# Performance work log

Measured on AMD Instinct MI355X. Metric: run time of the kernel, lower is better.

## Reference

```python
import jax, jax.numpy as jnp
import numpy as np

B, T, F, U = 64, 512, 32, 64
EPS = 1e-3  # keras LayerNormalization default epsilon


def _ln(x, g, b):
    m = jnp.mean(x, axis=-1, keepdims=True)
    v = jnp.var(x, axis=-1, keepdims=True)
    return (x - m) / jnp.sqrt(v + EPS) * g + b


def setup_inputs() -> dict:
    key = jax.random.key(0)
    ks = jax.random.split(key, 24)
    s = 0.05
    inp = {
        "x": jax.random.normal(ks[0], (B, T, F), dtype=jnp.float32),
        # per-feature GRNs, stacked over F (each sub-net has independent params)
        "W1": jax.random.normal(ks[1], (F, U), jnp.float32) * s,   # dense_1 (1->U)
        "b1": jnp.zeros((F, U), jnp.float32),
        "W2": jax.random.normal(ks[2], (F, U, U), jnp.float32) * s,  # dense_2 (U->U)
        "b2": jnp.zeros((F, U), jnp.float32),
        "Wg1": jax.random.normal(ks[3], (F, U, U), jnp.float32) * s,  # GLU linear
        "bg1": jnp.zeros((F, U), jnp.float32),
        "Wg2": jax.random.normal(ks[4], (F, U, U), jnp.float32) * s,  # GLU gate
        "bg2": jnp.zeros((F, U), jnp.float32),
        "Wp": jax.random.normal(ks[5], (F, U), jnp.float32) * s,   # project (1->U)
        "bp": jnp.zeros((F, U), jnp.float32),
        "gamma": jnp.ones((F, U), jnp.float32),
        "beta": jnp.zeros((F, U), jnp.float32),
        # weights GRN (F -> F, no projection since in_dim == units == F)
        "w1w": jax.random.normal(ks[6], (F, F), jnp.float32) * s,
        "b1w": jnp.zeros((F,), jnp.float32),
        "w2w": jax.random.normal(ks[7], (F, F), jnp.float32) * s,
        "b2w": jnp.zeros((F,), jnp.float32),
        "wg1w": jax.random.normal(ks[8], (F, F), jnp.float32) * s,
        "bg1w": jnp.zeros((F,), jnp.float32),
        "wg2w": jax.random.normal(ks[9], (F, F), jnp.float32) * s,
        "bg2w": jnp.zeros((F,), jnp.float32),
        "gammaw": jnp.ones((F,), jnp.float32),
        "betaw": jnp.zeros((F,), jnp.float32),
    }
    return inp


def reference(x, W1, b1, W2, b2, Wg1, bg1, Wg2, bg2, Wp, bp, gamma, beta,
              w1w, b1w, w2w, b2w, wg1w, bg1w, wg2w, bg2w, gammaw, betaw):
    # ---- variable weights GRN on flattened features (input dim F == units F, no projection) ----
    h = jax.nn.elu(jnp.einsum('btf,fg->btg', x, w1w) + b1w)
    h = jnp.einsum('btf,fg->btg', h, w2w) + b2w
    g = (jnp.einsum('btf,fg->btg', h, wg1w) + bg1w) * jax.nn.sigmoid(
        jnp.einsum('btf,fg->btg', h, wg2w) + bg2w)
    w = _ln(g + x, gammaw, betaw)
    w = jax.nn.softmax(w, axis=-1)  # [B,T,F]

    # ---- per-feature GRNs, batched over F (scalar input per feature) ----
    xe = x[..., None]                                   # [B,T,F,1]
    res = xe * Wp + bp                                  # project residual [B,T,F,U]
    h = jax.nn.elu(xe * W1 + b1)                        # dense_1 [B,T,F,U]
    h = jnp.einsum('btfu,fuv->btfv', h, W2) + b2        # dense_2
    g = (jnp.einsum('btfu,fuv->btfv', h, Wg1) + bg1) * jax.nn.sigmoid(
        jnp.einsum('btfu,fuv->btfv', h, Wg2) + bg2)     # GLU
    y = _ln(g + res, gamma, beta)                       # [B,T,F,U]

    out = jnp.einsum('btfu,btf->btu', y, w)             # softmax-weighted sum over features
    return out, w
```

## Files before the change

### kernel.cpp

```cpp
#include <hip/hip_runtime.h>
#include <hip/hip_bf16.h>


typedef float f4      __attribute__((ext_vector_type(4)));
typedef float f32x4   __attribute__((ext_vector_type(4)));
typedef short bf16x8  __attribute__((ext_vector_type(8)));
typedef unsigned short u16x4 __attribute__((ext_vector_type(4)));
typedef unsigned short u16x8 __attribute__((ext_vector_type(8)));

#define N_ROWS 32768
#define F_DIM  32
#define U_DIM  64
#define RPB    32
#define NTHR   256
#define NBLK   (N_ROWS / RPB)

#define X_OFF   0
#define WT_OFF  4608
#define R1_OFF  7168
#define H2_OFF  24576
#define SMEM_BYTES 33792

__device__ __forceinline__ unsigned short bfu(float x) {
  union { __hip_bfloat16 h; unsigned short u; } c;
  c.h = __float2bfloat16(x);
  return c.u;
}
__device__ __forceinline__ float bf2f(unsigned short u) {
  union { float f; unsigned v; } c; c.v = ((unsigned)u) << 16; return c.f;
}

__global__ __launch_bounds__(256) void vsn_prep(
    const float* __restrict__ W2,  const float* __restrict__ Wg1, const float* __restrict__ Wg2,
    const float* __restrict__ W1,  const float* __restrict__ b1,  const float* __restrict__ b2,
    const float* __restrict__ bg1, const float* __restrict__ bg2,
    const float* __restrict__ Wp,  const float* __restrict__ bp,
    const float* __restrict__ gamma_, const float* __restrict__ beta_,
    unsigned short* __restrict__ wtg, float* __restrict__ vect)
{
  const int t = threadIdx.x, blk = blockIdx.x;
  if (blk < 96) {
    const int m = blk >> 5, f = blk & 31;
    const float* src = (m == 0) ? W2 : (m == 1) ? Wg1 : Wg2;
    src += f * 4096;
    unsigned short* dst = wtg + (size_t)(m * 32 + f) * 4096;
    #pragma unroll
    for (int cc = 0; cc < 2; ++cc) {
      const int c  = t + cc * 256;
      const int nt = c >> 7;
      const int rr = c & 127;
      const int kt = rr >> 6;
      const int ln = rr & 63;
      const int lg = ln >> 4, lrr = ln & 15;
      const int v  = lrr + 16 * nt;
      const int u0 = 8 * lg + 32 * kt;
      u16x8 tmp;
      #pragma unroll
      for (int j = 0; j < 8; ++j) tmp[j] = bfu(src[(u0 + j) * 64 + v]);
      *(u16x8*)(dst + c * 8) = tmp;
    }
  } else {
    #pragma unroll
    for (int a = 0; a < 9; ++a) {
      const float* s = (a==0)?W1:(a==1)?b1:(a==2)?b2:(a==3)?bg1:(a==4)?bg2:
                       (a==5)?Wp:(a==6)?bp:(a==7)?gamma_:beta_;
      for (int i = t; i < 2048; i += 256)
        vect[(i >> 6) * 576 + a * 64 + (i & 63)] = s[i];
    }
  }
}

__global__ __launch_bounds__(NTHR, 4) void vsn_main(
    const float* __restrict__ x,
    const unsigned short* __restrict__ wtg,
    const float* __restrict__ vect,
    const float* __restrict__ w1w, const float* __restrict__ w2w,
    const float* __restrict__ wg1w, const float* __restrict__ wg2w,
    const float* __restrict__ b1w, const float* __restrict__ b2w,
    const float* __restrict__ bg1w, const float* __restrict__ bg2w,
    const float* __restrict__ gammaw, const float* __restrict__ betaw,
    float* __restrict__ out, float* __restrict__ wout)
{
  __shared__ __align__(16) char smem[SMEM_BYTES];
  const int t  = threadIdx.x;
  const int r0 = blockIdx.x * RPB;

  float* xt  = (float*)(smem + X_OFF);
  unsigned short* wtlb = (unsigned short*)(smem + WT_OFF);
  float* vst = (float*)(smem + R1_OFF);
  f4*   cmb4 = (f4*)(smem + R1_OFF + 9216);
  unsigned short* h2b = (unsigned short*)(smem + H2_OFF);
  float* wAl = (float*)(smem + R1_OFF);
  float* vAl = (float*)(smem + R1_OFF + 16384);
  float* hex = (float*)(smem + H2_OFF);

  const int wid  = t >> 6;
  const int lane = t & 63;
  const int lr   = lane & 15;
  const int lg   = lane >> 4;
  const int fbase = (wid >> 1) * 16;
  const int rbase = (wid & 1) * 16;

  {
    f4 v = ((const f4*)(x + (size_t)r0 * F_DIM))[t];
    *((f4*)(xt + (t >> 3) * 36 + ((t & 7) << 2))) = v;
  }

  const f4* vect4 = (const f4*)vect;
  f4 rv0 = vect4[fbase * 144 + lane];
  f4 rv1 = vect4[fbase * 144 + 64 + lane];
  f4 rv2 = {};
  if (lane < 16) rv2 = vect4[fbase * 144 + 128 + lane];

  #pragma unroll
  for (int i = 0; i < 4; ++i) {
    int i4 = t + i * NTHR;
    int m = i4 >> 8, off = (i4 & 255) << 2;
    const float* src = (m == 0) ? w1w : (m == 1) ? w2w : (m == 2) ? wg1w : wg2w;
    *(f4*)(wAl + m * 1024 + off) = *((const f4*)(src + off));
  }
  if (t < 48) {
    int m = t >> 3, off = (t & 7) << 2;
    const float* src = (m==0)?b1w:(m==1)?b2w:(m==2)?bg1w:(m==3)?bg2w:(m==4)?gammaw:betaw;
    *(f4*)(vAl + m * 32 + off) = *((const f4*)(src + off));
  }
  __syncthreads();

  {
    const int ar = t >> 3;
    const int g0 = (t & 7) << 2;

    float hacc[4];
    #pragma unroll
    for (int j = 0; j < 4; ++j) hacc[j] = vAl[0 * 32 + g0 + j];
    #pragma unroll
    for (int ff = 0; ff < 32; ++ff) {
      float xv = xt[ar * 36 + ff];
      f4 w0 = *(const f4*)(wAl + 0 * 1024 + ff * 32 + g0);
      #pragma unroll
      for (int j = 0; j < 4; ++j) hacc[j] += xv * w0[j];
    }
    #pragma unroll
    for (int j = 0; j < 4; ++j) { float z = hacc[j]; hacc[j] = z > 0.f ? z : (__expf(z) - 1.f); }
    *(f4*)(hex + ar * 36 + g0) = (f4){hacc[0], hacc[1], hacc[2], hacc[3]};
    __syncthreads();

    float h2acc[4];
    #pragma unroll
    for (int j = 0; j < 4; ++j) h2acc[j] = vAl[1 * 32 + g0 + j];
    #pragma unroll
    for (int ff = 0; ff < 32; ++ff) {
      float hv = hex[ar * 36 + ff];
      f4 w0 = *(const f4*)(wAl + 1 * 1024 + ff * 32 + g0);
      #pragma unroll
      for (int j = 0; j < 4; ++j) h2acc[j] += hv * w0[j];
    }
    __syncthreads();
    *(f4*)(hex + ar * 36 + g0) = (f4){h2acc[0], h2acc[1], h2acc[2], h2acc[3]};
    __syncthreads();

    float aacc[4], bacc[4];
    #pragma unroll
    for (int j = 0; j < 4; ++j) { aacc[j] = vAl[2 * 32 + g0 + j]; bacc[j] = vAl[3 * 32 + g0 + j]; }
    #pragma unroll
    for (int ff = 0; ff < 32; ++ff) {
      float hv = hex[ar * 36 + ff];
      f4 wa0 = *(const f4*)(wAl + 2 * 1024 + ff * 32 + g0);
      f4 wb0 = *(const f4*)(wAl + 3 * 1024 + ff * 32 + g0);
      #pragma unroll
      for (int j = 0; j < 4; ++j) { aacc[j] += hv * wa0[j]; bacc[j] += hv * wb0[j]; }
    }
    float zz[4];
    #pragma unroll
    for (int j = 0; j < 4; ++j) {
      float sg = __builtin_amdgcn_rcpf(1.f + __expf(-bacc[j]));
      zz[j] = aacc[j] * sg + xt[ar * 36 + g0 + j];
    }
    __syncthreads();
    *(f4*)(hex + ar * 36 + g0) = (f4){zz[0], zz[1], zz[2], zz[3]};
    __syncthreads();

    float s1 = 0.f, s2 = 0.f;
    #pragma unroll
    for (int ff = 0; ff < 32; ++ff) { float z = hex[ar * 36 + ff]; s1 += z; s2 += z * z; }
    float mA = s1 * 0.03125f;
    float vA = s2 * 0.03125f - mA * mA;
    float rsA = __builtin_amdgcn_rsqf(vA + 1e-3f);
    float mx = -1e30f;
    #pragma unroll
    for (int ff = 0; ff < 32; ++ff) {
      float y = (hex[ar * 36 + ff] - mA) * rsA * vAl[4 * 32 + ff] + vAl[5 * 32 + ff];
      mx = fmaxf(mx, y);
    }
    float es = 0.f;
    #pragma unroll
    for (int ff = 0; ff < 32; ++ff) {
      float y = (hex[ar * 36 + ff] - mA) * rsA * vAl[4 * 32 + ff] + vAl[5 * 32 + ff];
      es += __expf(y - mx);
    }
    float inv = __builtin_amdgcn_rcpf(es);
    float wv4[4];
    u16x4 wu;
    #pragma unroll
    for (int j = 0; j < 4; ++j) {
      float y = (hex[ar * 36 + g0 + j] - mA) * rsA * vAl[4 * 32 + g0 + j] + vAl[5 * 32 + g0 + j];
      wv4[j] = __expf(y - mx) * inv;
      wu[j] = bfu(wv4[j]);
    }
    *(u16x4*)(wtlb + ar * 40 + g0) = wu;
    *(f4*)(wout + (size_t)(r0 + ar) * 32 + g0) = (f4){wv4[0], wv4[1], wv4[2], wv4[3]};
    __syncthreads();
  }

  f4* vst4 = ((f4*)vst) + wid * 144;
  float* vsc = vst + wid * 576;
  unsigned short* h2w = h2b + wid * (16 * 72);

  vst4[lane] = rv0; vst4[64 + lane] = rv1;
  if (lane < 16) vst4[128 + lane] = rv2;

  const bf16x8* wf = (const bf16x8*)wtg;

  f32x4 acc[4];
  #pragma unroll
  for (int nt = 0; nt < 4; ++nt) acc[nt] = (f32x4){0.f, 0.f, 0.f, 0.f};

  for (int i = 0; i < 16; ++i) {
    const int f = fbase + i;

    const int base0 = (0 * 32 + f) * 512 + lane;
    bf16x8 bfr[8];
    #pragma unroll
    for (int nt = 0; nt < 4; ++nt)
      #pragma unroll
      for (int kt = 0; kt < 2; ++kt)
        bfr[nt * 2 + kt] = wf[base0 + nt * 128 + kt * 64];

    const float s_ = xt[(rbase + lr) * 36 + f];
    bf16x8 afr[2];
    #pragma unroll
    for (int kt = 0; kt < 2; ++kt) {
      const int u0 = 8 * lg + 32 * kt;
      f4 wa  = *(const f4*)(vsc + u0);
      f4 wb_ = *(const f4*)(vsc + u0 + 4);
      f4 ba  = *(const f4*)(vsc + 64 + u0);
      f4 bb_ = *(const f4*)(vsc + 64 + u0 + 4);
      bf16x8 af;
      #pragma unroll
      for (int j = 0; j < 4; ++j) {
        float h = s_ * wa[j] + ba[j];
        h = h > 0.f ? h : (__expf(h) - 1.f);
        af[j] = (short)bfu(h);
      }
      #pragma unroll
      for (int j = 0; j < 4; ++j) {
        float h = s_ * wb_[j] + bb_[j];
        h = h > 0.f ? h : (__expf(h) - 1.f);
        af[4 + j] = (short)bfu(h);
      }
      afr[kt] = af;
    }

    f32x4 c1[4];
    #pragma unroll
    for (int nt = 0; nt < 4; ++nt) {
      c1[nt] = (f32x4){0.f, 0.f, 0.f, 0.f};
      #pragma unroll
      for (int kt = 0; kt < 2; ++kt)
        c1[nt] = __builtin_amdgcn_mfma_f32_16x16x32_bf16(afr[kt], bfr[nt * 2 + kt], c1[nt], 0, 0, 0);
    }

    #pragma unroll
    for (int nt = 0; nt < 4; ++nt) {
      const float b2v = vsc[2 * 64 + lr + 16 * nt];
      #pragma unroll
      for (int rg = 0; rg < 4; ++rg)
        h2w[(4 * lg + rg) * 72 + lr + 16 * nt] = bfu(c1[nt][rg] + b2v);
    }

    const int base1 = (1 * 32 + f) * 512 + lane;
    bf16x8 bfa[8];
    #pragma unroll
    for (int nt = 0; nt < 4; ++nt)
      #pragma unroll
      for (int kt = 0; kt < 2; ++kt)
        bfa[nt * 2 + kt] = wf[base1 + nt * 128 + kt * 64];

    asm volatile("s_waitcnt lgkmcnt(0)" ::: "memory");
    __builtin_amdgcn_sched_barrier(0);

    bf16x8 a2[2];
    #pragma unroll
    for (int kt = 0; kt < 2; ++kt)
      a2[kt] = *(const bf16x8*)(h2w + lr * 72 + 8 * lg + 32 * kt);

    f32x4 ca[4], cb[4];
    #pragma unroll
    for (int nt = 0; nt < 4; ++nt) {
      ca[nt] = (f32x4){0.f,0.f,0.f,0.f};
      #pragma unroll
      for (int kt = 0; kt < 2; ++kt)
        ca[nt] = __builtin_amdgcn_mfma_f32_16x16x32_bf16(a2[kt], bfa[nt * 2 + kt], ca[nt], 0, 0, 0);
    }

    const int base2 = (2 * 32 + f) * 512 + lane;
    bf16x8 bfb[8];
    #pragma unroll
    for (int nt = 0; nt < 4; ++nt)
      #pragma unroll
      for (int kt = 0; kt < 2; ++kt)
        bfb[nt * 2 + kt] = wf[base2 + nt * 128 + kt * 64];
    #pragma unroll
    for (int nt = 0; nt < 4; ++nt) {
      cb[nt] = (f32x4){0.f,0.f,0.f,0.f};
      #pragma unroll
      for (int kt = 0; kt < 2; ++kt)
        cb[nt] = __builtin_amdgcn_mfma_f32_16x16x32_bf16(a2[kt], bfb[nt * 2 + kt], cb[nt], 0, 0, 0);
    }

    if (i < 15) {
      rv0 = vect4[(f + 1) * 144 + lane];
      rv1 = vect4[(f + 1) * 144 + 64 + lane];
      if (lane < 16) rv2 = vect4[(f + 1) * 144 + 128 + lane];
    }

    float xr[4], wr[4];
    #pragma unroll
    for (int rg = 0; rg < 4; ++rg) {
      const int rl = rbase + 4 * lg + rg;
      xr[rg] = xt[rl * 36 + f];
      wr[rg] = bf2f(wtlb[rl * 40 + f]);
    }
    float zf[4][4];
    float s1[4] = {0.f,0.f,0.f,0.f}, s2[4] = {0.f,0.f,0.f,0.f};
    #pragma unroll
    for (int nt = 0; nt < 4; ++nt) {
      const int u = lr + 16 * nt;
      const float bg1v = vsc[3 * 64 + u], bg2v = vsc[4 * 64 + u];
      const float wpv  = vsc[5 * 64 + u], bpv  = vsc[6 * 64 + u];
      #pragma unroll
      for (int rg = 0; rg < 4; ++rg) {
        float a = ca[nt][rg] + bg1v;
        float b = cb[nt][rg] + bg2v;
        float sg = __builtin_amdgcn_rcpf(1.f + __expf(-b));
        float z = a * sg + (xr[rg] * wpv + bpv);
        zf[nt][rg] = z;
        s1[rg] += z;
        s2[rg] += z * z;
      }
    }
    #pragma unroll
    for (int rg = 0; rg < 4; ++rg) {
      #pragma unroll
      for (int m = 1; m < 16; m <<= 1) {
        s1[rg] += __shfl_xor(s1[rg], m, 64);
        s2[rg] += __shfl_xor(s2[rg], m, 64);
      }
    }
    float mn[4], rs[4];
    #pragma unroll
    for (int rg = 0; rg < 4; ++rg) {
      mn[rg] = s1[rg] * 0.015625f;
      float var = s2[rg] * 0.015625f - mn[rg] * mn[rg];
      rs[rg] = __builtin_amdgcn_rsqf(var + 1e-3f);
    }
    #pragma unroll
    for (int nt = 0; nt < 4; ++nt) {
      const int u = lr + 16 * nt;
      const float gav = vsc[7 * 64 + u], bev = vsc[8 * 64 + u];
      #pragma unroll
      for (int rg = 0; rg < 4; ++rg) {
        float y = (zf[nt][rg] - mn[rg]) * rs[rg] * gav + bev;
        acc[nt][rg] += y * wr[rg];
      }
    }

    if (i < 15) {
      vst4[lane] = rv0; vst4[64 + lane] = rv1;
      if (lane < 16) vst4[128 + lane] = rv2;
    }
  }

  if (wid >= 2) {
    #pragma unroll
    for (int nt = 0; nt < 4; ++nt)
      cmb4[(wid - 2) * 256 + nt * 64 + lane] = acc[nt];
  }
  __syncthreads();
  if (wid < 2) {
    #pragma unroll
    for (int nt = 0; nt < 4; ++nt) {
      f4 o = acc[nt] + cmb4[wid * 256 + nt * 64 + lane];
      #pragma unroll
      for (int rg = 0; rg < 4; ++rg) {
        const int row = r0 + rbase + 4 * lg + rg;
        out[(size_t)row * U_DIM + lr + 16 * nt] = o[rg];
      }
    }
  }
}

extern "C" void kernel_launch(void* const* d_in, const int* in_sizes, int n_in,
                              void* d_out, int out_size, void* d_ws, size_t ws_size,
                              hipStream_t stream)
{
  (void)in_sizes; (void)n_in; (void)out_size; (void)ws_size;
  const float* x    = (const float*)d_in[0];
  const float* W1   = (const float*)d_in[1];
  const float* b1   = (const float*)d_in[2];
  const float* W2   = (const float*)d_in[3];
  const float* b2   = (const float*)d_in[4];
  const float* Wg1  = (const float*)d_in[5];
  const float* bg1  = (const float*)d_in[6];
  const float* Wg2  = (const float*)d_in[7];
  const float* bg2  = (const float*)d_in[8];
  const float* Wp   = (const float*)d_in[9];
  const float* bp   = (const float*)d_in[10];
  const float* gm   = (const float*)d_in[11];
  const float* bt   = (const float*)d_in[12];
  const float* w1w  = (const float*)d_in[13];
  const float* b1w  = (const float*)d_in[14];
  const float* w2w  = (const float*)d_in[15];
  const float* b2w  = (const float*)d_in[16];
  const float* wg1w = (const float*)d_in[17];
  const float* bg1w = (const float*)d_in[18];
  const float* wg2w = (const float*)d_in[19];
  const float* bg2w = (const float*)d_in[20];
  const float* gmw  = (const float*)d_in[21];
  const float* btw  = (const float*)d_in[22];

  unsigned short* wtg = (unsigned short*)d_ws;
  float* vect = (float*)((char*)d_ws + 786432);

  float* out  = (float*)d_out;
  float* wout = out + (size_t)N_ROWS * U_DIM;

  vsn_prep<<<97, 256, 0, stream>>>(W2, Wg1, Wg2, W1, b1, b2, bg1, bg2, Wp, bp, gm, bt, wtg, vect);
  vsn_main<<<NBLK, NTHR, 0, stream>>>(x, wtg, vect, w1w, w2w, wg1w, wg2w,
                                      b1w, b2w, bg1w, bg2w, gmw, btw, out, wout);
}
```

Before: 207.3 us.

## Halve rows per block, keep dense_2 output in registers, repack per-feature vectors

Each block now handles 16 rows instead of 32, with each of the four waves owning 8 features over all 16 rows, and occupancy is raised to 8 blocks per SM. The dense_2 MFMA is transposed and the Wg1/Wg2 weight layout is permuted so the h2 result can feed the GLU MFMAs straight from registers, removing the LDS round trip and waitcnt barrier. Per-feature bias and LN vectors are interleaved for vectorized loads, the LN and weighted-sum math is folded into fewer FMAs, and the final cross-wave reduction writes coalesced f4 rows. In exchange, per-row weight fetches from global/L2 double because fewer rows share each feature's weights, and the prep kernel now uses more blocks.

Measured after the change: 329.8 us. +59.1%, slower.

```diff
diff --git a/kernel.cpp b/kernel.cpp
--- a/kernel.cpp
+++ b/kernel.cpp
@@ -3,23 +3,24 @@
 
 
 typedef float f4      __attribute__((ext_vector_type(4)));
+typedef float f2      __attribute__((ext_vector_type(2)));
 typedef float f32x4   __attribute__((ext_vector_type(4)));
 typedef short bf16x8  __attribute__((ext_vector_type(8)));
-typedef unsigned short u16x4 __attribute__((ext_vector_type(4)));
 typedef unsigned short u16x8 __attribute__((ext_vector_type(8)));
 
 #define N_ROWS 32768
 #define F_DIM  32
 #define U_DIM  64
-#define RPB    32
+#define RPB    16
 #define NTHR   256
 #define NBLK   (N_ROWS / RPB)
 
 #define X_OFF   0
-#define WT_OFF  4608
-#define R1_OFF  7168
-#define H2_OFF  24576
-#define SMEM_BYTES 33792
+#define WT_OFF  2304
+#define PW_OFF  3584
+#define VA_OFF  11776
+#define HX_OFF  12544
+#define SMEM_BYTES 19968
 
 __device__ __forceinline__ unsigned short bfu(float x) {
   union { __hip_bfloat16 h; unsigned short u; } c;
@@ -39,38 +40,49 @@
     unsigned short* __restrict__ wtg, float* __restrict__ vect)
 {
   const int t = threadIdx.x, blk = blockIdx.x;
-  if (blk < 96) {
-    const int m = blk >> 5, f = blk & 31;
+  if (blk < 192) {
+    const int m = blk >> 6;
+    const int f = (blk >> 1) & 31;
+    const int half = blk & 1;
     const float* src = (m == 0) ? W2 : (m == 1) ? Wg1 : Wg2;
     src += f * 4096;
-    unsigned short* dst = wtg + (size_t)(m * 32 + f) * 4096;
-    #pragma unroll
-    for (int cc = 0; cc < 2; ++cc) {
-      const int c  = t + cc * 256;
-      const int nt = c >> 7;
-      const int rr = c & 127;
-      const int kt = rr >> 6;
-      const int ln = rr & 63;
-      const int lg = ln >> 4, lrr = ln & 15;
-      const int v  = lrr + 16 * nt;
-      const int u0 = 8 * lg + 32 * kt;
-      u16x8 tmp;
-      #pragma unroll
-      for (int j = 0; j < 8; ++j) tmp[j] = bfu(src[(u0 + j) * 64 + v]);
-      *(u16x8*)(dst + c * 8) = tmp;
-    }
+    const int c  = half * 256 + t;
+    const int nt = c >> 7;
+    const int rr = c & 127;
+    const int kt = rr >> 6;
+    const int ln = rr & 63;
+    const int g  = ln >> 4, lrr = ln & 15;
+    const int uo = lrr + 16 * nt;
+    u16x8 tmp;
+    if (m == 0) {
+      #pragma unroll
+      for (int j = 0; j < 8; ++j)
+        tmp[j] = bfu(src[(8 * g + 32 * kt + j) * 64 + uo]);
+    } else {
+      #pragma unroll
+      for (int j = 0; j < 8; ++j)
+        tmp[j] = bfu(src[(4 * g + (j & 3) + 16 * (j >> 2) + 32 * kt) * 64 + uo]);
+    }
+    *(u16x8*)(wtg + ((size_t)(m * 32 + f) * 512 + c) * 8) = tmp;
   } else {
-    #pragma unroll
-    for (int a = 0; a < 9; ++a) {
-      const float* s = (a==0)?W1:(a==1)?b1:(a==2)?b2:(a==3)?bg1:(a==4)?bg2:
-                       (a==5)?Wp:(a==6)?bp:(a==7)?gamma_:beta_;
-      for (int i = t; i < 2048; i += 256)
-        vect[(i >> 6) * 576 + a * 64 + (i & 63)] = s[i];
+    const int h = blk - 192;
+    for (int i = h * 1024 + t; i < (h + 1) * 1024; i += 256) {
+      const int f = i >> 6, u = i & 63;
+      float* vf = vect + f * 576;
+      vf[u]              = W1[i];
+      vf[64 + u]         = b1[i];
+      vf[128 + u]        = b2[i];
+      vf[192 + u * 4 + 0] = bg1[i];
+      vf[192 + u * 4 + 1] = bg2[i];
+      vf[192 + u * 4 + 2] = Wp[i];
+      vf[192 + u * 4 + 3] = bp[i];
+      vf[448 + u * 2 + 0] = gamma_[i];
+      vf[448 + u * 2 + 1] = beta_[i];
     }
   }
 }
 
-__global__ __launch_bounds__(NTHR, 4) void vsn_main(
+__global__ __launch_bounds__(NTHR, 8) void vsn_main(
     const float* __restrict__ x,
     const unsigned short* __restrict__ wtg,
     const float* __restrict__ vect,
@@ -87,21 +99,17 @@
 
   float* xt  = (float*)(smem + X_OFF);
   unsigned short* wtlb = (unsigned short*)(smem + WT_OFF);
-  float* vst = (float*)(smem + R1_OFF);
-  f4*   cmb4 = (f4*)(smem + R1_OFF + 9216);
-  unsigned short* h2b = (unsigned short*)(smem + H2_OFF);
-  float* wAl = (float*)(smem + R1_OFF);
-  float* vAl = (float*)(smem + R1_OFF + 16384);
-  float* hex = (float*)(smem + H2_OFF);
+  float* wA  = (float*)(smem + PW_OFF);
+  float* vAl = (float*)(smem + VA_OFF);
+  float* hex = (float*)(smem + HX_OFF);
 
   const int wid  = t >> 6;
   const int lane = t & 63;
   const int lr   = lane & 15;
   const int lg   = lane >> 4;
-  const int fbase = (wid >> 1) * 16;
-  const int rbase = (wid & 1) * 16;
-
-  {
+  const int fbase = wid * 8;
+
+  if (t < 128) {
     f4 v = ((const f4*)(x + (size_t)r0 * F_DIM))[t];
     *((f4*)(xt + (t >> 3) * 36 + ((t & 7) << 2))) = v;
   }
@@ -113,11 +121,11 @@
   if (lane < 16) rv2 = vect4[fbase * 144 + 128 + lane];
 
   #pragma unroll
-  for (int i = 0; i < 4; ++i) {
+  for (int i = 0; i < 2; ++i) {
     int i4 = t + i * NTHR;
     int m = i4 >> 8, off = (i4 & 255) << 2;
-    const float* src = (m == 0) ? w1w : (m == 1) ? w2w : (m == 2) ? wg1w : wg2w;
-    *(f4*)(wAl + m * 1024 + off) = *((const f4*)(src + off));
+    const float* src = m ? w2w : w1w;
+    *(f4*)(wA + m * 1024 + off) = *((const f4*)(src + off));
   }
   if (t < 48) {
     int m = t >> 3, off = (t & 7) << 2;
@@ -127,57 +135,58 @@
   __syncthreads();
 
   {
-    const int ar = t >> 3;
-    const int g0 = (t & 7) << 2;
-
-    float hacc[4];
-    #pragma unroll
-    for (int j = 0; j < 4; ++j) hacc[j] = vAl[0 * 32 + g0 + j];
+    const int ar = t >> 4;
+    const int g0 = (t & 15) << 1;
+
+    f2 hacc = { vAl[g0], vAl[g0 + 1] };
     #pragma unroll
     for (int ff = 0; ff < 32; ++ff) {
       float xv = xt[ar * 36 + ff];
-      f4 w0 = *(const f4*)(wAl + 0 * 1024 + ff * 32 + g0);
-      #pragma unroll
-      for (int j = 0; j < 4; ++j) hacc[j] += xv * w0[j];
-    }
-    #pragma unroll
-    for (int j = 0; j < 4; ++j) { float z = hacc[j]; hacc[j] = z > 0.f ? z : (__expf(z) - 1.f); }
-    *(f4*)(hex + ar * 36 + g0) = (f4){hacc[0], hacc[1], hacc[2], hacc[3]};
-    __syncthreads();
-
-    float h2acc[4];
-    #pragma unroll
-    for (int j = 0; j < 4; ++j) h2acc[j] = vAl[1 * 32 + g0 + j];
+      f2 w0 = *(const f2*)(wA + ff * 32 + g0);
+      hacc.x += xv * w0.x; hacc.y += xv * w0.y;
+    }
+    hacc.x = hacc.x > 0.f ? hacc.x : (__expf(hacc.x) - 1.f);
+    hacc.y = hacc.y > 0.f ? hacc.y : (__expf(hacc.y) - 1.f);
+    *(f2*)(hex + ar * 36 + g0) = hacc;
+    __syncthreads();
+
+    f2 h2acc = { vAl[32 + g0], vAl[32 + g0 + 1] };
     #pragma unroll
     for (int ff = 0; ff < 32; ++ff) {
       float hv = hex[ar * 36 + ff];
-      f4 w0 = *(const f4*)(wAl + 1 * 1024 + ff * 32 + g0);
-      #pragma unroll
-      for (int j = 0; j < 4; ++j) h2acc[j] += hv * w0[j];
-    }
-    __syncthreads();
-    *(f4*)(hex + ar * 36 + g0) = (f4){h2acc[0], h2acc[1], h2acc[2], h2acc[3]};
-    __syncthreads();
-
-    float aacc[4], bacc[4];
-    #pragma unroll
-    for (int j = 0; j < 4; ++j) { aacc[j] = vAl[2 * 32 + g0 + j]; bacc[j] = vAl[3 * 32 + g0 + j]; }
+      f2 w0 = *(const f2*)(wA + 1024 + ff * 32 + g0);
+      h2acc.x += hv * w0.x; h2acc.y += hv * w0.y;
+    }
+    __syncthreads();
+    *(f2*)(hex + ar * 36 + g0) = h2acc;
+    #pragma unroll
+    for (int i = 0; i < 2; ++i) {
+      int i4 = t + i * NTHR;
+      int m = i4 >> 8, off = (i4 & 255) << 2;
+      const float* src = m ? wg2w : wg1w;
+      *(f4*)(wA + m * 1024 + off) = *((const f4*)(src + off));
+    }
+    __syncthreads();
+
+    f2 aacc = { vAl[64 + g0], vAl[64 + g0 + 1] };
+    f2 bacc = { vAl[96 + g0], vAl[96 + g0 + 1] };
     #pragma unroll
     for (int ff = 0; ff < 32; ++ff) {
       float hv = hex[ar * 36 + ff];
-      f4 wa0 = *(const f4*)(wAl + 2 * 1024 + ff * 32 + g0);
-      f4 wb0 = *(const f4*)(wAl + 3 * 1024 + ff * 32 + g0);
-      #pragma unroll
-      for (int j = 0; j < 4; ++j) { aacc[j] += hv * wa0[j]; bacc[j] += hv * wb0[j]; }
-    }
-    float zz[4];
-    #pragma unroll
-    for (int j = 0; j < 4; ++j) {
-      float sg = __builtin_amdgcn_rcpf(1.f + __expf(-bacc[j]));
-      zz[j] = aacc[j] * sg + xt[ar * 36 + g0 + j];
-    }
-    __syncthreads();
-    *(f4*)(hex + ar * 36 + g0) = (f4){zz[0], zz[1], zz[2], zz[3]};
+      f2 wa0 = *(const f2*)(wA + ff * 32 + g0);
+      f2 wb0 = *(const f2*)(wA + 1024 + ff * 32 + g0);
+      aacc.x += hv * wa0.x; aacc.y += hv * wa0.y;
+      bacc.x += hv * wb0.x; bacc.y += hv * wb0.y;
+    }
+    f2 zz;
+    {
+      float sgx = __builtin_amdgcn_rcpf(1.f + __expf(-bacc.x));
+      float sgy = __builtin_amdgcn_rcpf(1.f + __expf(-bacc.y));
+      zz.x = aacc.x * sgx + xt[ar * 36 + g0];
+      zz.y = aacc.y * sgy + xt[ar * 36 + g0 + 1];
+    }
+    __syncthreads();
+    *(f2*)(hex + ar * 36 + g0) = zz;
     __syncthreads();
 
     float s1 = 0.f, s2 = 0.f;
@@ -189,32 +198,26 @@
     float mx = -1e30f;
     #pragma unroll
     for (int ff = 0; ff < 32; ++ff) {
-      float y = (hex[ar * 36 + ff] - mA) * rsA * vAl[4 * 32 + ff] + vAl[5 * 32 + ff];
+      float y = (hex[ar * 36 + ff] - mA) * rsA * vAl[128 + ff] + vAl[160 + ff];
       mx = fmaxf(mx, y);
     }
     float es = 0.f;
     #pragma unroll
     for (int ff = 0; ff < 32; ++ff) {
-      float y = (hex[ar * 36 + ff] - mA) * rsA * vAl[4 * 32 + ff] + vAl[5 * 32 + ff];
+      float y = (hex[ar * 36 + ff] - mA) * rsA * vAl[128 + ff] + vAl[160 + ff];
       es += __expf(y - mx);
     }
     float inv = __builtin_amdgcn_rcpf(es);
-    float wv4[4];
-    u16x4 wu;
-    #pragma unroll
-    for (int j = 0; j < 4; ++j) {
-      float y = (hex[ar * 36 + g0 + j] - mA) * rsA * vAl[4 * 32 + g0 + j] + vAl[5 * 32 + g0 + j];
-      wv4[j] = __expf(y - mx) * inv;
-      wu[j] = bfu(wv4[j]);
-    }
-    *(u16x4*)(wtlb + ar * 40 + g0) = wu;
-    *(f4*)(wout + (size_t)(r0 + ar) * 32 + g0) = (f4){wv4[0], wv4[1], wv4[2], wv4[3]};
-    __syncthreads();
-  }
-
-  f4* vst4 = ((f4*)vst) + wid * 144;
-  float* vsc = vst + wid * 576;
-  unsigned short* h2w = h2b + wid * (16 * 72);
+    float w0 = __expf((hex[ar * 36 + g0] - mA) * rsA * vAl[128 + g0] + vAl[160 + g0] - mx) * inv;
+    float w1_ = __expf((hex[ar * 36 + g0 + 1] - mA) * rsA * vAl[128 + g0 + 1] + vAl[160 + g0 + 1] - mx) * inv;
+    unsigned wu = (unsigned)bfu(w0) | ((unsigned)bfu(w1_) << 16);
+    *(unsigned*)(wtlb + ar * 40 + g0) = wu;
+    *(f2*)(wout + (size_t)(r0 + ar) * 32 + g0) = (f2){w0, w1_};
+    __syncthreads();
+  }
+
+  f4* vst4 = ((f4*)(smem + PW_OFF)) + wid * 144;
+  float* vsc = (float*)(smem + PW_OFF) + wid * 576;
 
   vst4[lane] = rv0; vst4[64 + lane] = rv1;
   if (lane < 16) vst4[128 + lane] = rv2;
@@ -225,18 +228,18 @@
   #pragma unroll
   for (int nt = 0; nt < 4; ++nt) acc[nt] = (f32x4){0.f, 0.f, 0.f, 0.f};
 
-  for (int i = 0; i < 16; ++i) {
+  for (int i = 0; i < 8; ++i) {
     const int f = fbase + i;
 
     const int base0 = (0 * 32 + f) * 512 + lane;
-    bf16x8 bfr[8];
+    bf16x8 w2f[8];
     #pragma unroll
     for (int nt = 0; nt < 4; ++nt)
       #pragma unroll
       for (int kt = 0; kt < 2; ++kt)
-        bfr[nt * 2 + kt] = wf[base0 + nt * 128 + kt * 64];
-
-    const float s_ = xt[(rbase + lr) * 36 + f];
+        w2f[nt * 2 + kt] = wf[base0 + nt * 128 + kt * 64];
+
+    const float s_ = xt[lr * 36 + f];
     bf16x8 afr[2];
     #pragma unroll
     for (int kt = 0; kt < 2; ++kt) {
@@ -267,15 +270,25 @@
       c1[nt] = (f32x4){0.f, 0.f, 0.f, 0.f};
       #pragma unroll
       for (int kt = 0; kt < 2; ++kt)
-        c1[nt] = __builtin_amdgcn_mfma_f32_16x16x32_bf16(afr[kt], bfr[nt * 2 + kt], c1[nt], 0, 0, 0);
-    }
-
-    #pragma unroll
-    for (int nt = 0; nt < 4; ++nt) {
-      const float b2v = vsc[2 * 64 + lr + 16 * nt];
-      #pragma unroll
-      for (int rg = 0; rg < 4; ++rg)
-        h2w[(4 * lg + rg) * 72 + lr + 16 * nt] = bfu(c1[nt][rg] + b2v);
+        c1[nt] = __builtin_amdgcn_mfma_f32_16x16x32_bf16(w2f[nt * 2 + kt], afr[kt], c1[nt], 0, 0, 0);
+    }
+
+    f4 b2q[4];
+    #pragma unroll
+    for (int kt = 0; kt < 2; ++kt)
+      #pragma unroll
+      for (int n2 = 0; n2 < 2; ++n2)
+        b2q[n2 + 2 * kt] = *(const f4*)(vsc + 128 + 4 * lg + 16 * n2 + 32 * kt);
+    bf16x8 a2[2];
+    #pragma unroll
+    for (int kt = 0; kt < 2; ++kt) {
+      bf16x8 af;
+      #pragma unroll
+      for (int j = 0; j < 8; ++j) {
+        const int q = (j >> 2) + 2 * kt;
+        af[j] = (short)bfu(c1[q][j & 3] + b2q[q][j & 3]);
+      }
+      a2[kt] = af;
     }
 
     const int base1 = (1 * 32 + f) * 512 + lane;
@@ -285,15 +298,6 @@
       #pragma unroll
       for (int kt = 0; kt < 2; ++kt)
         bfa[nt * 2 + kt] = wf[base1 + nt * 128 + kt * 64];
-
-    asm volatile("s_waitcnt lgkmcnt(0)" ::: "memory");
-    __builtin_amdgcn_sched_barrier(0);
-
-    bf16x8 a2[2];
-    #pragma unroll
-    for (int kt = 0; kt < 2; ++kt)
-      a2[kt] = *(const bf16x8*)(h2w + lr * 72 + 8 * lg + 32 * kt);
-
     f32x4 ca[4], cb[4];
     #pragma unroll
     for (int nt = 0; nt < 4; ++nt) {
@@ -318,7 +322,7 @@
         cb[nt] = __builtin_amdgcn_mfma_f32_16x16x32_bf16(a2[kt], bfb[nt * 2 + kt], cb[nt], 0, 0, 0);
     }
 
-    if (i < 15) {
+    if (i < 7) {
       rv0 = vect4[(f + 1) * 144 + lane];
       rv1 = vect4[(f + 1) * 144 + 64 + lane];
       if (lane < 16) rv2 = vect4[(f + 1) * 144 + 128 + lane];
@@ -327,7 +331,7 @@
     float xr[4], wr[4];
     #pragma unroll
     for (int rg = 0; rg < 4; ++rg) {
-      const int rl = rbase + 4 * lg + rg;
+      const int rl = 4 * lg + rg;
       xr[rg] = xt[rl * 36 + f];
       wr[rg] = bf2f(wtlb[rl * 40 + f]);
     }
@@ -336,14 +340,13 @@
     #pragma unroll
     for (int nt = 0; nt < 4; ++nt) {
       const int u = lr + 16 * nt;
-      const float bg1v = vsc[3 * 64 + u], bg2v = vsc[4 * 64 + u];
-      const float wpv  = vsc[5 * 64 + u], bpv  = vsc[6 * 64 + u];
+      f4 Q = *(const f4*)(vsc + 192 + u * 4);
       #pragma unroll
       for (int rg = 0; rg < 4; ++rg) {
-        float a = ca[nt][rg] + bg1v;
-        float b = cb[nt][rg] + bg2v;
+        float a = ca[nt][rg] + Q[0];
+        float b = cb[nt][rg] + Q[1];
         float sg = __builtin_amdgcn_rcpf(1.f + __expf(-b));
-        float z = a * sg + (xr[rg] * wpv + bpv);
+        float z = a * sg + (xr[rg] * Q[2] + Q[3]);
         zf[nt][rg] = z;
         s1[rg] += z;
         s2[rg] += z * z;
@@ -357,46 +360,44 @@
         s2[rg] += __shfl_xor(s2[rg], m, 64);
       }
     }
-    float mn[4], rs[4];
+    float rswr[4], nc2[4];
     #pragma unroll
     for (int rg = 0; rg < 4; ++rg) {
-      mn[rg] = s1[rg] * 0.015625f;
-      float var = s2[rg] * 0.015625f - mn[rg] * mn[rg];
-      rs[rg] = __builtin_amdgcn_rsqf(var + 1e-3f);
+      float mn = s1[rg] * 0.015625f;
+      float var = s2[rg] * 0.015625f - mn * mn;
+      float rs = __builtin_amdgcn_rsqf(var + 1e-3f);
+      rswr[rg] = rs * wr[rg];
+      nc2[rg]  = -mn * rswr[rg];
     }
     #pragma unroll
     for (int nt = 0; nt < 4; ++nt) {
       const int u = lr + 16 * nt;
-      const float gav = vsc[7 * 64 + u], bev = vsc[8 * 64 + u];
+      f2 G = *(const f2*)(vsc + 448 + u * 2);
       #pragma unroll
       for (int rg = 0; rg < 4; ++rg) {
-        float y = (zf[nt][rg] - mn[rg]) * rs[rg] * gav + bev;
-        acc[nt][rg] += y * wr[rg];
-      }
-    }
-
-    if (i < 15) {
+        float tm = rswr[rg] * zf[nt][rg] + nc2[rg];
+        acc[nt][rg] += G.x * tm + G.y * wr[rg];
+      }
+    }
+
+    if (i < 7) {
       vst4[lane] = rv0; vst4[64 + lane] = rv1;
       if (lane < 16) vst4[128 + lane] = rv2;
     }
   }
 
-  if (wid >= 2) {
-    #pragma unroll
-    for (int nt = 0; nt < 4; ++nt)
-      cmb4[(wid - 2) * 256 + nt * 64 + lane] = acc[nt];
-  }
   __syncthreads();
-  if (wid < 2) {
-    #pragma unroll
-    for (int nt = 0; nt < 4; ++nt) {
-      f4 o = acc[nt] + cmb4[wid * 256 + nt * 64 + lane];
-      #pragma unroll
-      for (int rg = 0; rg < 4; ++rg) {
-        const int row = r0 + rbase + 4 * lg + rg;
-        out[(size_t)row * U_DIM + lr + 16 * nt] = o[rg];
-      }
-    }
+  float* cmb = (float*)(smem + PW_OFF);
+  #pragma unroll
+  for (int nt = 0; nt < 4; ++nt)
+    #pragma unroll
+    for (int rg = 0; rg < 4; ++rg)
+      cmb[wid * 1024 + (4 * lg + rg) * 64 + lr + 16 * nt] = acc[nt][rg];
+  __syncthreads();
+  {
+    const f4* cmb4 = (const f4*)cmb;
+    f4 o = cmb4[t] + cmb4[256 + t] + cmb4[512 + t] + cmb4[768 + t];
+    ((f4*)(out + (size_t)r0 * U_DIM))[t] = o;
   }
 }
 
@@ -435,7 +436,7 @@
   float* out  = (float*)d_out;
   float* wout = out + (size_t)N_ROWS * U_DIM;
 
-  vsn_prep<<<97, 256, 0, stream>>>(W2, Wg1, Wg2, W1, b1, b2, bg1, bg2, Wp, bp, gm, bt, wtg, vect);
+  vsn_prep<<<194, 256, 0, stream>>>(W2, Wg1, Wg2, W1, b1, b2, bg1, bg2, Wp, bp, gm, bt, wtg, vect);
   vsn_main<<<NBLK, NTHR, 0, stream>>>(x, wtg, vect, w1w, w2w, wg1w, wg2w,
                                       b1w, b2w, bg1w, bg2w, gmw, btw, out, wout);
 }
```
